# Kernel optimization log

Hardware: AMD Instinct MI355X
Metric: run time of the kernel (lower is better)

## Reference

```python
import jax, jax.numpy as jnp
import numpy as np

B, S, D = 2, 2048, 1024
NH, NKV, DH = 16, 4, 64
DFF, E, K, DE = 4096, 8, 2, 1024
CHUNK = 512
THETA = 10000.0
ROPE_PERIOD = 4  # int(1/(1-0.75))


def rmsnorm(x, gamma):
    den = jnp.sqrt(jnp.mean(x * x, axis=-1, keepdims=True) + 1e-6)
    return x / den * gamma


def apply_rope(x, base):
    # x: [b, s, h, d]
    s, d = x.shape[1], x.shape[3]
    m = jnp.arange(s, dtype=x.dtype)[:, None]                    # [s,1]
    i = jnp.arange(0, d, 2, dtype=x.dtype)
    theta = jnp.power(jnp.asarray(base, x.dtype), -i / d)        # [d/2]
    ang = (m * theta)[None, :, None, :]                          # [1,s,1,d/2]
    cos, sin = jnp.cos(ang), jnp.sin(ang)
    x1, x2 = x[..., 0::2], x[..., 1::2]
    r1 = x1 * cos - x2 * sin
    r2 = x1 * sin + x2 * cos
    return jnp.stack([r1, r2], axis=-1).reshape(x.shape)


def setup_inputs() -> dict:
    key = jax.random.key(0)
    ks = jax.random.split(key, 16)
    sc = 0.02
    inp = {
        "x": jax.random.normal(ks[0], (B, S, D), jnp.float32),
        "idx": 1,
        "gamma1": jnp.ones((D,), jnp.float32),
        "gamma2": jnp.ones((D,), jnp.float32),
        "q_gamma": jnp.ones((DH,), jnp.float32),
        "k_gamma": jnp.ones((DH,), jnp.float32),
        "w_q": jax.random.normal(ks[1], (D, NH * DH), jnp.float32) * sc,
        "w_k": jax.random.normal(ks[2], (D, NKV * DH), jnp.float32) * sc,
        "w_v": jax.random.normal(ks[3], (D, NKV * DH), jnp.float32) * sc,
        "w_o": jax.random.normal(ks[4], (D, D), jnp.float32) * sc,
        "w_router": jax.random.normal(ks[5], (D, E), jnp.float32) * sc,
        "sh_wg": jax.random.normal(ks[6], (D, DE), jnp.float32) * sc,
        "sh_wu": jax.random.normal(ks[7], (D, DE), jnp.float32) * sc,
        "sh_wd": jax.random.normal(ks[8], (DE, D), jnp.float32) * sc,
        "e_wg": jax.random.normal(ks[9], (E, D, DE), jnp.float32) * sc,
        "e_wu": jax.random.normal(ks[10], (E, D, DE), jnp.float32) * sc,
        "e_wd": jax.random.normal(ks[11], (E, DE, D), jnp.float32) * sc,
    }
    return inp


def reference(x, idx, gamma1, gamma2, q_gamma, k_gamma, w_q, w_k, w_v, w_o,
              w_router, sh_wg, sh_wu, sh_wd, e_wg, e_wu, e_wd):
    b, s, d = x.shape
    x_res = x
    h = rmsnorm(x, gamma1)

    # --- attention ---
    q = (h @ w_q).reshape(b, s, NH, DH)
    k = (h @ w_k).reshape(b, s, NKV, DH)
    v = (h @ w_v).reshape(b, s, NKV, DH)
    q = rmsnorm(q, q_gamma)
    k = rmsnorm(k, k_gamma)

    is_rope = (idx + 1) % ROPE_PERIOD != 0
    if is_rope:
        q = apply_rope(q, THETA)
        k = apply_rope(k, THETA)

    n_rep = NH // NKV
    k = jnp.repeat(k, n_rep, axis=2)  # [b,s,NH,DH]
    v = jnp.repeat(v, n_rep, axis=2)

    scores = jnp.einsum('bqhd,bkhd->bhqk', q, k) / np.sqrt(DH).astype(np.float32)

    pos = jnp.arange(s)
    if is_rope:
        same_chunk = (pos[:, None] // CHUNK) == (pos[None, :] // CHUNK)
        allowed = same_chunk & (pos[None, :] <= pos[:, None])
    else:
        allowed = pos[None, :] <= pos[:, None]
    scores = jnp.where(allowed[None, None], scores, -jnp.inf)
    attn = jax.nn.softmax(scores, axis=-1)
    out = jnp.einsum('bhqk,bkhd->bqhd', attn, v).reshape(b, s, d)
    x = out @ w_o + x_res

    # --- FFN ---
    x_res = x
    h = rmsnorm(x, gamma2)
    if idx % 2 == 0:
        raise NotImplementedError('dense layer path not exercised (idx odd)')
    # MoE: router + top-k combine (dense-weights formulation, same math)
    hf = h.reshape(-1, d)                           # [T, D]
    T = hf.shape[0]
    probs = jax.nn.softmax(hf @ w_router, axis=-1)  # [T, E]
    topw, topi = jax.lax.top_k(probs, K)
    topw = topw / jnp.sum(topw, axis=-1, keepdims=True)
    dense_w = jnp.zeros((T, E), hf.dtype).at[jnp.arange(T)[:, None], topi].add(topw)

    # shared expert
    sh = (jax.nn.silu(hf @ sh_wg) * (hf @ sh_wu)) @ sh_wd

    # all experts densely, weighted combine (zero-weight experts contribute 0)
    g = jax.nn.silu(jnp.einsum('td,edf->etf', hf, e_wg))
    u = jnp.einsum('td,edf->etf', hf, e_wu)
    eo = jnp.einsum('etf,efd->etd', g * u, e_wd)    # [E, T, D]
    moe = jnp.einsum('te,etd->td', dense_w, eo) + sh

    return moe.reshape(b, s, d) + x_res
```

## Files before the change

### kernel.cpp

```cpp
#include <hip/hip_runtime.h>
#include <hip/hip_bf16.h>

#define TS    2048
#define TT    4096
#define TCHUNK 512

typedef __bf16 bf16;
typedef __bf16 bf16x8 __attribute__((ext_vector_type(8)));
typedef __bf16 bf16x4 __attribute__((ext_vector_type(4)));
typedef float  f32x4  __attribute__((ext_vector_type(4)));

#define QPL ((size_t)TT*1024)
#define KPL ((size_t)TT*256)
#define VPL ((size_t)8*64*TS)
#define APL ((size_t)TT*1024)
#define H1PL ((size_t)TT*1024)

__device__ __forceinline__ f32x4 mfma16(bf16x8 a, bf16x8 b, f32x4 c){
  return __builtin_amdgcn_mfma_f32_16x16x32_bf16(a, b, c, 0, 0, 0);
}
__device__ __forceinline__ void gload_lds16(const void* g, void* lds){
  __builtin_amdgcn_global_load_lds(
      (const __attribute__((address_space(1))) unsigned int*)g,
      (__attribute__((address_space(3))) unsigned int*)lds, 16, 0, 0);
}
__device__ __forceinline__ void split2f(float x, bf16& h, bf16& m){
  h = (bf16)x; m = (bf16)(x - (float)h);
}

__global__ __launch_bounds__(256) void tcvt2_all_k(const float* __restrict__ wq, const float* __restrict__ wk,
                                                   const float* __restrict__ wv, const float* __restrict__ wo,
                                                   bf16* __restrict__ wqkv2, bf16* __restrict__ wo2){
  int z = blockIdx.z;
  const float* src; bf16* dst; int C; long pl, doff;
  if (z==0){ src=wq; dst=wqkv2; C=1024; pl=(long)1536*1024; doff=0; }
  else if (z==1){ src=wk; dst=wqkv2; C=256; pl=(long)1536*1024; doff=(long)1024*1024; }
  else if (z==2){ src=wv; dst=wqkv2; C=256; pl=(long)1536*1024; doff=(long)1280*1024; }
  else { src=wo; dst=wo2; C=1024; pl=(long)1024*1024; doff=0; }
  int c0 = blockIdx.x*32;
  if (c0 >= C) return;
  __shared__ float tile[32][33];
  int r0 = blockIdx.y*32;
  int tx = threadIdx.x, ty = threadIdx.y;
  #pragma unroll
  for (int i=0;i<4;i++)
    tile[ty+i*8][tx] = src[(size_t)(r0+ty+i*8)*C + c0+tx];
  __syncthreads();
  #pragma unroll
  for (int i=0;i<4;i++){
    float v = tile[tx][ty+i*8];
    bf16 h,m; split2f(v,h,m);
    size_t o = doff + (size_t)(c0+ty+i*8)*1024 + r0+tx;
    dst[o] = h; dst[pl + o] = m;
  }
}

__global__ __launch_bounds__(256) void tcvt_moe_k(const float* __restrict__ shwg, const float* __restrict__ shwu,
                                                  const float* __restrict__ shwd, const float* __restrict__ ewg,
                                                  const float* __restrict__ ewu, const float* __restrict__ ewd,
                                                  bf16* __restrict__ shwgu, bf16* __restrict__ shwd_t,
                                                  bf16* __restrict__ ewgu, bf16* __restrict__ ewd_t){
  int z = blockIdx.z;
  const float* src; bf16* dst; int mode;
  if (z==0){ src=shwg; dst=shwgu; mode=0; }
  else if (z==1){ src=shwu; dst=shwgu; mode=1; }
  else if (z==2){ src=shwd; dst=shwd_t; mode=2; }
  else if (z<11){ int e=z-3;  src=ewg+(size_t)e*1048576; dst=ewgu+(size_t)e*2097152; mode=0; }
  else if (z<19){ int e=z-11; src=ewu+(size_t)e*1048576; dst=ewgu+(size_t)e*2097152; mode=1; }
  else          { int e=z-19; src=ewd+(size_t)e*1048576; dst=ewd_t+(size_t)e*1048576; mode=2; }
  __shared__ float tile[32][33];
  int r0 = blockIdx.y*32, c0 = blockIdx.x*32;
  int tx = threadIdx.x, ty = threadIdx.y;
  #pragma unroll
  for (int i=0;i<4;i++)
    tile[ty+i*8][tx] = src[(size_t)(r0+ty+i*8)*1024 + c0+tx];
  __syncthreads();
  #pragma unroll
  for (int i=0;i<4;i++){
    int c = c0+ty+i*8;
    int orow = (mode==2) ? c : ((c>>4)*32 + (c&15) + (mode==1?16:0));
    dst[(size_t)orow*1024 + r0+tx] = (bf16)tile[tx][ty+i*8];
  }
}

__global__ __launch_bounds__(256) void rmsnorm2_k(const float* __restrict__ x, const float* __restrict__ g,
                                                  bf16* __restrict__ o2){
  int row = blockIdx.x, tid = threadIdx.x, wid = tid>>6, lane = tid&63;
  f32x4 v = ((const f32x4*)(x + (size_t)row*1024))[tid];
  float ss = v[0]*v[0]+v[1]*v[1]+v[2]*v[2]+v[3]*v[3];
  #pragma unroll
  for (int m=1;m<64;m<<=1) ss += __shfl_xor(ss, m);
  __shared__ float red[4];
  if (lane==0) red[wid] = ss;
  __syncthreads();
  float tot = red[0]+red[1]+red[2]+red[3];
  float inv = rsqrtf(tot*(1.f/1024.f) + 1e-6f);
  f32x4 gv = ((const f32x4*)g)[tid];
  #pragma unroll
  for (int i=0;i<4;i++){
    float val = v[i]*inv*gv[i];
    bf16 h,m; split2f(val,h,m);
    size_t idx = (size_t)row*1024 + tid*4 + i;
    o2[idx] = h; o2[H1PL + idx] = m;
  }
}

template<int OUT, int GATHER, int GROUPED>
__global__ __launch_bounds__(256) void gemm_k(
    const bf16* __restrict__ Aptr, int lda,
    const bf16* __restrict__ Bt, long bMatStride,
    void* __restrict__ Cout, int ldc,
    const float* __restrict__ resid,
    const int* __restrict__ gidx,
    const int* __restrict__ grpBase,
    const int* __restrict__ grpCnt,
    int M, int K){
  int tid = threadIdx.x;
  int wid = tid >> 6, lane = tid & 63;
  int lr = lane & 15, lg = lane >> 4;
  int e = blockIdx.z;
  int base = GROUPED ? grpBase[e] : 0;
  int cnt  = GROUPED ? grpCnt[e]  : M;
  int m0, bn0;
  if (GROUPED){
    m0 = blockIdx.y * 128;
    bn0 = blockIdx.x * 128;
  } else {
    int gx = gridDim.x;
    int bid = blockIdx.y*gx + blockIdx.x;
    int cpx = (gx*gridDim.y)>>3;
    int swz = (bid&7)*cpx + (bid>>3);
    m0 = (swz/gx) * 128;
    bn0 = (swz%gx) * 128;
  }
  if (m0 >= cnt) return;
  const bf16* Bte = Bt + (size_t)e * bMatStride;

  __shared__ __align__(16) bf16 As[128*32];
  __shared__ __align__(16) bf16 Bs[128*32];

  int rA0 = tid >> 2, colA = (tid & 3) * 8;
  long arow[2], brow[2];
  #pragma unroll
  for (int i=0;i<2;i++){
    int r = rA0 + i*64;
    int ar = m0 + r; if (ar > cnt-1) ar = cnt-1;
    arow[i] = GATHER ? (long)gidx[base + ar] : (long)(base + ar);
    brow[i] = bn0 + r;
  }

  f32x4 zero4 = {0.f,0.f,0.f,0.f};
  f32x4 acc[4][4];
  #pragma unroll
  for (int m=0;m<4;m++)
    #pragma unroll
    for (int n=0;n<4;n++) acc[m][n] = zero4;

  char* ldsA = (char*)As + wid*1024;
  char* ldsB = (char*)Bs + wid*1024;
  int wr = (wid>>1)*64, wc = (wid&1)*64;

  for (int k0 = 0; k0 < K; k0 += 32){
    #pragma unroll
    for (int i=0;i<2;i++){
      gload_lds16(Aptr + arow[i]*lda + k0 + colA, ldsA + i*4096);
      gload_lds16(Bte  + brow[i]*K   + k0 + colA, ldsB + i*4096);
    }
    asm volatile("s_waitcnt vmcnt(0)" ::: "memory");
    __syncthreads();
    bf16x8 af[4], bfr[4];
    #pragma unroll
    for (int m=0;m<4;m++) af[m]  = *(const bf16x8*)&As[(wr + m*16 + lr)*32 + lg*8];
    #pragma unroll
    for (int n=0;n<4;n++) bfr[n] = *(const bf16x8*)&Bs[(wc + n*16 + lr)*32 + lg*8];
    #pragma unroll
    for (int m=0;m<4;m++)
      #pragma unroll
      for (int n=0;n<4;n++)
        acc[m][n] = mfma16(af[m], bfr[n], acc[m][n]);
    __syncthreads();
  }
  #pragma unroll
  for (int m=0;m<4;m++){
    #pragma unroll
    for (int j=0;j<4;j++){
      int gr = m0 + wr + m*16 + lg*4 + j;
      if (gr < cnt){
        size_t orow = (size_t)(base + gr);
        if (OUT==2){
          #pragma unroll
          for (int np=0;np<2;np++){
            float gv = acc[m][2*np][j], uv = acc[m][2*np+1][j];
            float ov = gv * uv / (1.f + __expf(-gv));
            int f = ((bn0+wc)>>1) + np*16 + lr;
            ((bf16*)Cout)[orow*ldc + f] = (bf16)ov;
          }
        } else {
          #pragma unroll
          for (int n=0;n<4;n++){
            int gc = bn0 + wc + n*16 + lr;
            float v = acc[m][n][j];
            if (OUT==1){
              ((bf16*)Cout)[orow*ldc + gc] = (bf16)v;
            } else {
              ((float*)Cout)[orow*ldc + gc] = v + resid[orow*ldc + gc];
            }
          }
        }
      }
    }
  }
}

template<int RESID>
__global__ __launch_bounds__(256) void gemm2_k(
    const bf16* __restrict__ A2, long aPL, int lda,
    const bf16* __restrict__ B2, long bPL, int K,
    float* __restrict__ C, int ldc,
    const float* __restrict__ resid){
  int tid = threadIdx.x;
  int wid = tid >> 6, lane = tid & 63;
  int lr = lane & 15, lg = lane >> 4;
  int gx = gridDim.x;
  int bid = blockIdx.y*gx + blockIdx.x;
  int cpx = (gx*gridDim.y)>>3;
  int swz = (bid&7)*cpx + (bid>>3);
  int m0 = (swz/gx) * 128;
  int bn0 = (swz%gx) * 128;

  __shared__ __align__(16) bf16 As[2*128*32];
  __shared__ __align__(16) bf16 Bs[2*128*32];

  int rA0 = tid >> 2, colA = (tid & 3) * 8;
  f32x4 zero4 = {0.f,0.f,0.f,0.f};
  f32x4 acc[4][4];
  #pragma unroll
  for (int m=0;m<4;m++)
    #pragma unroll
    for (int n=0;n<4;n++) acc[m][n] = zero4;

  int wr = (wid>>1)*64, wc = (wid&1)*64;

  for (int k0 = 0; k0 < K; k0 += 32){
    #pragma unroll
    for (int p=0;p<2;p++){
      #pragma unroll
      for (int i=0;i<2;i++){
        int r = rA0 + i*64;
        gload_lds16(A2 + (size_t)p*aPL + (size_t)(m0 + r)*lda + k0 + colA,
                    (char*)As + p*8192 + wid*1024 + i*4096);
        gload_lds16(B2 + (size_t)p*bPL + (size_t)(bn0 + r)*K + k0 + colA,
                    (char*)Bs + p*8192 + wid*1024 + i*4096);
      }
    }
    asm volatile("s_waitcnt vmcnt(0)" ::: "memory");
    __syncthreads();
    bf16x8 af[2][4], bfr[2][4];
    #pragma unroll
    for (int p=0;p<2;p++){
      #pragma unroll
      for (int m=0;m<4;m++) af[p][m]  = *(const bf16x8*)&As[p*4096 + (wr + m*16 + lr)*32 + lg*8];
      #pragma unroll
      for (int n=0;n<4;n++) bfr[p][n] = *(const bf16x8*)&Bs[p*4096 + (wc + n*16 + lr)*32 + lg*8];
    }
    #pragma unroll
    for (int m=0;m<4;m++)
      #pragma unroll
      for (int n=0;n<4;n++){
        f32x4 a = acc[m][n];
        a = mfma16(af[0][m], bfr[0][n], a);
        a = mfma16(af[0][m], bfr[1][n], a);
        a = mfma16(af[1][m], bfr[0][n], a);
        a = mfma16(af[1][m], bfr[1][n], a);
        acc[m][n] = a;
      }
    __syncthreads();
  }
  #pragma unroll
  for (int m=0;m<4;m++){
    #pragma unroll
    for (int j=0;j<4;j++){
      size_t orow = (size_t)(m0 + wr + m*16 + lg*4 + j);
      #pragma unroll
      for (int n=0;n<4;n++){
        int gc = bn0 + wc + n*16 + lr;
        float v = acc[m][n][j];
        if (RESID) v += resid[orow*ldc + gc];
        C[orow*ldc + gc] = v;
      }
    }
  }
}

__global__ __launch_bounds__(256) void rope2_k(const float* __restrict__ qkv, bf16* __restrict__ Q2,
                                               bf16* __restrict__ K2, const int* __restrict__ idxp,
                                               const float* __restrict__ qg, const float* __restrict__ kg){
  int tid = threadIdx.x, wid = tid>>6, lane = tid&63;
  int u = blockIdx.x*4 + wid;
  int t = u / 20, r = u % 20;
  bool isq = (r < 16);
  int srcOff = isq ? r*64 : 1024 + (r-16)*64;
  float val = qkv[(size_t)t*1536 + srcOff + lane];
  float ss = val*val;
  #pragma unroll
  for (int m=1;m<64;m<<=1) ss += __shfl_xor(ss, m);
  float inv = rsqrtf(ss*(1.f/64.f) + 1e-6f);
  const float* gm = isq ? qg : kg;
  val = val * inv * gm[lane];
  bool rope = ((idxp[0] + 1) % 4) != 0;
  if (rope){
    int s = t & (TS-1);
    float fi = (float)(lane & ~1);
    float theta = (float)exp((double)fi * -0.14391156831212787);
    float ang = (float)s * theta;
    float sn, cs;
    sincosf(ang, &sn, &cs);
    float other = __shfl_xor(val, 1);
    val = (lane & 1) ? (other*sn + val*cs) : (val*cs - other*sn);
  }
  bf16 h,m2; split2f(val,h,m2);
  if (isq){
    size_t base = (size_t)t*1024 + r*64 + lane;
    Q2[base] = h; Q2[QPL + base] = m2;
  } else {
    size_t base = (size_t)t*256 + (r-16)*64 + lane;
    K2[base] = h; K2[KPL + base] = m2;
  }
}

__global__ __launch_bounds__(256) void vtrans2_k(const float* __restrict__ src, bf16* __restrict__ dst){
  __shared__ float tile[32][33];
  int z = blockIdx.z;
  const float* s = src + (size_t)(z>>2)*((size_t)TS*1536) + (z&3)*64 + 1280;
  int r0 = blockIdx.y*32, c0 = blockIdx.x*32;
  int tx = threadIdx.x, ty = threadIdx.y;
  #pragma unroll
  for (int i=0;i<4;i++)
    tile[ty+i*8][tx] = s[(size_t)(r0+ty+i*8)*1536 + c0+tx];
  __syncthreads();
  size_t zb = (size_t)z*(64*TS);
  #pragma unroll
  for (int i=0;i<4;i++){
    float v = tile[tx][ty+i*8];
    bf16 h,m; split2f(v,h,m);
    size_t o = zb + (size_t)(c0+ty+i*8)*TS + r0+tx;
    dst[o] = h; dst[VPL + o] = m;
  }
}

__global__ __launch_bounds__(256) void attn2_k(const bf16* __restrict__ Q2, const bf16* __restrict__ K2,
                                               const bf16* __restrict__ V2, bf16* __restrict__ A2,
                                               const int* __restrict__ idxp){
  int tid = threadIdx.x, wid = tid>>6, lane = tid&63;
  int lr = lane&15, lg = lane>>4;
  int flat = (blockIdx.z*gridDim.y + blockIdx.y)*gridDim.x + blockIdx.x;
  int swz = (flat&7)*128 + (flat>>3);
  int qt = swz & 31, h = (swz>>5)&15, b = swz>>9;
  int kvh = h >> 2;
  int q0 = qt*64;
  bool rope = ((idxp[0]+1) % 4) != 0;
  int kstart = rope ? (q0 / TCHUNK) * TCHUNK : 0;
  int ntiles = (q0 + 64 - kstart) >> 5;

  __shared__ __align__(16) bf16 Ks[2*32*64];
  __shared__ __align__(16) bf16 Vs[2*64*32];
  __shared__ __align__(16) bf16 Ps[4][2][16*32];

  bf16x8 qf[2][2];
  {
    size_t qrow = (size_t)(b*TS + q0 + wid*16 + lr);
    #pragma unroll
    for (int p=0;p<2;p++)
      #pragma unroll
      for (int kf=0;kf<2;kf++)
        qf[p][kf] = *(const bf16x8*)&Q2[(size_t)p*QPL + qrow*1024 + h*64 + kf*32 + lg*8];
  }

  int krow = tid>>3;
  int kcb  = (tid&7) ^ (krow&7);
  int vrow = tid>>2;
  int vcb  = tid&3;

  f32x4 o[4];
  f32x4 zero4 = {0.f,0.f,0.f,0.f};
  #pragma unroll
  for (int n=0;n<4;n++) o[n] = zero4;
  float mrow[4], lrow[4];
  #pragma unroll
  for (int j=0;j<4;j++){ mrow[j] = -1e30f; lrow[j] = 0.f; }

  for (int kt=0; kt<ntiles; kt++){
    int kt0 = kstart + kt*32;
    #pragma unroll
    for (int p=0;p<2;p++){
      gload_lds16(K2 + (size_t)p*KPL + ((size_t)(b*TS + kt0 + krow))*256 + kvh*64 + kcb*8,
                  (char*)Ks + p*4096 + wid*1024);
      gload_lds16(V2 + (size_t)p*VPL + ((size_t)((b*4 + kvh)*64 + vrow))*TS + kt0 + vcb*8,
                  (char*)Vs + p*4096 + wid*1024);
    }
    asm volatile("s_waitcnt vmcnt(0)" ::: "memory");
    __syncthreads();

    f32x4 sc[2];
    #pragma unroll
    for (int cf=0; cf<2; cf++){
      int r = cf*16 + lr;
      int sw = (lr&7) << 3;
      bf16x8 kh0 = *(const bf16x8*)&Ks[0*2048 + r*64 + (((lg  )<<3) ^ sw)];
      bf16x8 kh1 = *(const bf16x8*)&Ks[0*2048 + r*64 + (((lg+4)<<3) ^ sw)];
      bf16x8 km0 = *(const bf16x8*)&Ks[1*2048 + r*64 + (((lg  )<<3) ^ sw)];
      bf16x8 km1 = *(const bf16x8*)&Ks[1*2048 + r*64 + (((lg+4)<<3) ^ sw)];
      f32x4 a = zero4;
      a = mfma16(qf[0][0], kh0, a); a = mfma16(qf[0][1], kh1, a);
      a = mfma16(qf[0][0], km0, a); a = mfma16(qf[0][1], km1, a);
      a = mfma16(qf[1][0], kh0, a); a = mfma16(qf[1][1], kh1, a);
      a = mfma16(qf[1][0], km0, a); a = mfma16(qf[1][1], km1, a);
      sc[cf] = a;
    }
    #pragma unroll
    for (int j=0;j<4;j++){
      int qtok = q0 + wid*16 + lg*4 + j;
      float pmax = -1e30f;
      #pragma unroll
      for (int cf=0;cf<2;cf++){
        int ktok = kt0 + cf*16 + lr;
        float sv = (ktok <= qtok) ? sc[cf][j]*0.125f : -1e30f;
        sc[cf][j] = sv;
        pmax = fmaxf(pmax, sv);
      }
      #pragma unroll
      for (int m=1;m<16;m<<=1) pmax = fmaxf(pmax, __shfl_xor(pmax, m));
      float mnew = fmaxf(mrow[j], pmax);
      float corr = __expf(mrow[j]-mnew);
      float psum = 0.f;
      #pragma unroll
      for (int cf=0;cf<2;cf++){
        float p = __expf(sc[cf][j]-mnew);
        sc[cf][j] = p;
        psum += p;
      }
      #pragma unroll
      for (int m=1;m<16;m<<=1) psum += __shfl_xor(psum, m);
      lrow[j] = lrow[j]*corr + psum;
      mrow[j] = mnew;
      #pragma unroll
      for (int n=0;n<4;n++) o[n][j] *= corr;
      #pragma unroll
      for (int cf=0;cf<2;cf++){
        float p = sc[cf][j];
        bf16 ph = (bf16)p;
        bf16 pl = (bf16)(p - (float)ph);
        int pidx = (lg*4+j)*32 + cf*16 + lr;
        Ps[wid][0][pidx] = ph;
        Ps[wid][1][pidx] = pl;
      }
    }
    __syncthreads();
    bf16x8 pa0 = *(const bf16x8*)&Ps[wid][0][lr*32 + lg*8];
    bf16x8 pa1 = *(const bf16x8*)&Ps[wid][1][lr*32 + lg*8];
    #pragma unroll
    for (int n=0;n<4;n++){
      bf16x8 vh = *(const bf16x8*)&Vs[0*2048 + (n*16+lr)*32 + lg*8];
      bf16x8 vm = *(const bf16x8*)&Vs[1*2048 + (n*16+lr)*32 + lg*8];
      f32x4 a = o[n];
      a = mfma16(pa0, vh, a);
      a = mfma16(pa0, vm, a);
      a = mfma16(pa1, vh, a);
      a = mfma16(pa1, vm, a);
      o[n] = a;
    }
    __syncthreads();
  }
  #pragma unroll
  for (int j=0;j<4;j++){
    int qtok = q0 + wid*16 + lg*4 + j;
    float invl = 1.f / lrow[j];
    size_t rowb = ((size_t)(b*TS + qtok))*1024 + h*64;
    #pragma unroll
    for (int n=0;n<4;n++){
      float v = o[n][j]*invl;
      bf16 h2,m2; split2f(v,h2,m2);
      size_t oidx = rowb + n*16 + lr;
      A2[oidx] = h2; A2[APL + oidx] = m2;
    }
  }
}

__global__ __launch_bounds__(256) void rmsrouter_k(const float* __restrict__ x2, const float* __restrict__ g2,
                                                   const float* __restrict__ wr, bf16* __restrict__ h2,
                                                   int* __restrict__ topi, float* __restrict__ topw){
  int tid = threadIdx.x, wid = tid>>6, lane = tid&63;
  int t = blockIdx.x*4 + wid;
  const float* row = x2 + (size_t)t*1024;
  f32x4 xv[4];
  float ss = 0.f;
  #pragma unroll
  for (int j=0;j<4;j++){
    xv[j] = ((const f32x4*)row)[lane + j*64];
    ss += xv[j][0]*xv[j][0]+xv[j][1]*xv[j][1]+xv[j][2]*xv[j][2]+xv[j][3]*xv[j][3];
  }
  #pragma unroll
  for (int m=1;m<64;m<<=1) ss += __shfl_xor(ss, m);
  float inv = 1.f / sqrtf(ss*(1.f/1024.f) + 1e-6f);
  float a[8] = {0,0,0,0,0,0,0,0};
  #pragma unroll
  for (int j=0;j<4;j++){
    bf16x4 hb;
    #pragma unroll
    for (int c=0;c<4;c++){
      int d = (lane + j*64)*4 + c;
      float hv = xv[j][c]*inv*g2[d];
      hb[c] = (bf16)hv;
      f32x4 wa = ((const f32x4*)(wr + (size_t)d*8))[0];
      f32x4 wb = ((const f32x4*)(wr + (size_t)d*8))[1];
      a[0]+=hv*wa[0]; a[1]+=hv*wa[1]; a[2]+=hv*wa[2]; a[3]+=hv*wa[3];
      a[4]+=hv*wb[0]; a[5]+=hv*wb[1]; a[6]+=hv*wb[2]; a[7]+=hv*wb[3];
    }
    *(bf16x4*)(h2 + (size_t)t*1024 + (lane + j*64)*4) = hb;
  }
  #pragma unroll
  for (int e2=0;e2<8;e2++)
    #pragma unroll
    for (int m=1;m<64;m<<=1) a[e2] += __shfl_xor(a[e2], m);
  if (lane==0){
    int i0=0; float l0=a[0];
    #pragma unroll
    for (int e2=1;e2<8;e2++) if (a[e2] > l0){ l0=a[e2]; i0=e2; }
    int i1=-1; float l1=-1e30f;
    #pragma unroll
    for (int e2=0;e2<8;e2++){ if (e2==i0) continue; if (a[e2] > l1){ l1=a[e2]; i1=e2; } }
    float w0 = 1.f/(1.f + __expf(l1 - l0));
    topi[t*2]=i0; topi[t*2+1]=i1;
    topw[t*2]=w0; topw[t*2+1]=1.f-w0;
  }
}

__global__ __launch_bounds__(1024) void route_build_k(const int* __restrict__ topi, int* __restrict__ rowsb,
                                                      int* __restrict__ t2p, int* __restrict__ cntp,
                                                      int* __restrict__ basep){
  __shared__ int wcnt[16][8], wbase[16][8], wcur[16][8];
  int tid = threadIdx.x, w = tid>>6;
  if (tid < 128){ wcnt[tid>>3][tid&7]=0; wcur[tid>>3][tid&7]=0; }
  __syncthreads();
  for (int i=tid; i<TT*2; i+=1024) atomicAdd(&wcnt[w][topi[i]], 1);
  __syncthreads();
  if (tid==0){
    int run=0;
    for (int e=0;e<8;e++){
      basep[e]=run; int s=run;
      for (int ww=0;ww<16;ww++){ wbase[ww][e]=run; run+=wcnt[ww][e]; }
      cntp[e]=run-s;
    }
  }
  __syncthreads();
  for (int i=tid; i<TT*2; i+=1024){
    int e = topi[i];
    int p = wbase[w][e] + atomicAdd(&wcur[w][e], 1);
    rowsb[p] = i>>1;
    t2p[i] = p;
  }
}

__global__ void combine_k(const float* __restrict__ acc, const bf16* __restrict__ eo,
                          const float* __restrict__ topw, const int* __restrict__ t2p,
                          float* __restrict__ out){
  int i = blockIdx.x*256 + threadIdx.x;
  int t = i >> 8, c = (i & 255)*4;
  int p0 = t2p[t*2], p1 = t2p[t*2+1];
  float w0 = topw[t*2], w1 = topw[t*2+1];
  f32x4 a = *(const f32x4*)&acc[(size_t)t*1024 + c];
  bf16x4 e0 = *(const bf16x4*)&eo[(size_t)p0*1024 + c];
  bf16x4 e1 = *(const bf16x4*)&eo[(size_t)p1*1024 + c];
  f32x4 r;
  #pragma unroll
  for (int k=0;k<4;k++) r[k] = a[k] + w0*(float)e0[k] + w1*(float)e1[k];
  *(f32x4*)&out[(size_t)t*1024 + c] = r;
}

extern "C" void kernel_launch(void* const* d_in, const int* in_sizes, int n_in,
                              void* d_out, int out_size, void* d_ws, size_t ws_size,
                              hipStream_t stream){
  const float* x        = (const float*)d_in[0];
  const int*   idx      = (const int*)d_in[1];
  const float* gamma1   = (const float*)d_in[2];
  const float* gamma2   = (const float*)d_in[3];
  const float* qg       = (const float*)d_in[4];
  const float* kg       = (const float*)d_in[5];
  const float* w_q      = (const float*)d_in[6];
  const float* w_k      = (const float*)d_in[7];
  const float* w_v      = (const float*)d_in[8];
  const float* w_o      = (const float*)d_in[9];
  const float* w_router = (const float*)d_in[10];
  const float* sh_wg    = (const float*)d_in[11];
  const float* sh_wu    = (const float*)d_in[12];
  const float* sh_wd    = (const float*)d_in[13];
  const float* e_wg     = (const float*)d_in[14];
  const float* e_wu     = (const float*)d_in[15];
  const float* e_wd     = (const float*)d_in[16];
  float* out = (float*)d_out;

  char* ws = (char*)d_ws;
  size_t off = 0;
  auto alloc = [&](size_t n)->char*{ char* p = ws + off; off += (n + 255) & ~(size_t)255; return p; };

  const long PLQKV = (long)1536*1024;
  const long PLSQ  = (long)1024*1024;

  bf16* wqkv2  = (bf16*)alloc((size_t)2*1536*1024*2);
  bf16* wo2    = (bf16*)alloc((size_t)2*1024*1024*2);
  bf16* shwgu_t= (bf16*)alloc((size_t)2048*1024*2);
  bf16* shwd_t = (bf16*)alloc((size_t)1024*1024*2);
  bf16* ewgu_t = (bf16*)alloc((size_t)8*2048*1024*2);
  bf16* ewd_t  = (bf16*)alloc((size_t)8*1024*1024*2);
  bf16* h1s    = (bf16*)alloc((size_t)2*TT*1024*2);
  float* qkvraw= (float*)alloc((size_t)TT*1536*4);
  bf16* q2     = (bf16*)alloc((size_t)2*TT*1024*2);
  bf16* k2     = (bf16*)alloc((size_t)2*TT*256*2);
  bf16* v2     = (bf16*)alloc((size_t)2*8*64*TS*2);
  float* x2    = (float*)alloc((size_t)TT*1024*4);
  float* accb  = (float*)alloc((size_t)TT*1024*4);
  char* BUF2   = alloc((size_t)8192*1024*2);
  bf16* eo     = (bf16*)alloc((size_t)8192*1024*2);
  int*   topi  = (int*)alloc((size_t)TT*2*4);
  float* topw  = (float*)alloc((size_t)TT*2*4);
  int*   rowsb = (int*)alloc((size_t)TT*2*4);
  int*   t2p   = (int*)alloc((size_t)TT*2*4);
  int*   cntp  = (int*)alloc(256);
  int*   basep = (int*)alloc(256);
  (void)ws_size; (void)in_sizes; (void)n_in; (void)out_size;

  bf16* a2     = (bf16*)qkvraw;
  bf16* h2     = q2;
  bf16* shg    = (bf16*)BUF2;
  bf16* gu     = (bf16*)BUF2;

  dim3 tb(32,8);
  tcvt2_all_k<<<dim3(32,32,4), tb, 0, stream>>>(w_q, w_k, w_v, w_o, wqkv2, wo2);
  tcvt_moe_k<<<dim3(32,32,27), tb, 0, stream>>>(sh_wg, sh_wu, sh_wd, e_wg, e_wu, e_wd,
                                                shwgu_t, shwd_t, ewgu_t, ewd_t);

  rmsnorm2_k<<<TT, 256, 0, stream>>>(x, gamma1, h1s);
  gemm2_k<0><<<dim3(12,32,1), 256, 0, stream>>>(h1s, (long)H1PL, 1024, wqkv2, PLQKV, 1024,
                                                qkvraw, 1536, nullptr);
  rope2_k<<<TT*20/4, 256, 0, stream>>>(qkvraw, q2, k2, idx, qg, kg);
  vtrans2_k<<<dim3(2,64,8), tb, 0, stream>>>(qkvraw, v2);
  attn2_k<<<dim3(32,16,2), 256, 0, stream>>>(q2, k2, v2, a2, idx);
  gemm2_k<1><<<dim3(8,32,1), 256, 0, stream>>>(a2, (long)APL, 1024, wo2, PLSQ, 1024,
                                               x2, 1024, x);
  rmsrouter_k<<<TT/4, 256, 0, stream>>>(x2, gamma2, w_router, h2, topi, topw);
  route_build_k<<<1, 1024, 0, stream>>>(topi, rowsb, t2p, cntp, basep);
  gemm_k<2,0,0><<<dim3(16,32,1), 256, 0, stream>>>(h2,1024, shwgu_t,0, shg,1024,
                                                   nullptr, nullptr, nullptr, nullptr, TT, 1024);
  gemm_k<0,0,0><<<dim3(8,32,1), 256, 0, stream>>>(shg,1024, shwd_t,0, accb,1024,
                                                  x2, nullptr, nullptr, nullptr, TT, 1024);
  gemm_k<2,1,1><<<dim3(16,64,8), 256, 0, stream>>>(h2,1024, ewgu_t,(long)2048*1024, gu,1024,
                                                   nullptr, rowsb, basep, cntp, TT, 1024);
  gemm_k<1,0,1><<<dim3(8,64,8), 256, 0, stream>>>(gu,1024, ewd_t,(long)1024*1024, eo,1024,
                                                  nullptr, nullptr, basep, cntp, TT, 1024);
  combine_k<<<TT, 256, 0, stream>>>(accb, eo, topw, t2p, out);
}
```

Baseline: 429.9 us.

## Fold shared expert into grouped MoE GEMMs and drop low-order split MFMAs

Treats the shared expert as a ninth expert group covering all tokens: its weights sit after the routed experts, rowsb gains an identity segment, and the grouped GEMMs launch with nine z-slices. This removes two separate shared-expert GEMM launches and the fp32 accumulation buffer, and the combine kernel adds the shared output. Separately, it drops the lo*lo term of the split-bf16 products in the QKV/O GEMMs and both attention matmuls, cutting MFMA work at a small precision cost. The shared-expert output is now stored as bf16 instead of fp32 with the residual added, which adds rounding.

```diff
diff --git a/kernel.cpp b/kernel.cpp
--- a/kernel.cpp
+++ b/kernel.cpp
@@ -199,12 +199,7 @@
           #pragma unroll
           for (int n=0;n<4;n++){
             int gc = bn0 + wc + n*16 + lr;
-            float v = acc[m][n][j];
-            if (OUT==1){
-              ((bf16*)Cout)[orow*ldc + gc] = (bf16)v;
-            } else {
-              ((float*)Cout)[orow*ldc + gc] = v + resid[orow*ldc + gc];
-            }
+            ((bf16*)Cout)[orow*ldc + gc] = (bf16)acc[m][n][j];
           }
         }
       }
@@ -271,7 +266,6 @@
         a = mfma16(af[0][m], bfr[0][n], a);
         a = mfma16(af[0][m], bfr[1][n], a);
         a = mfma16(af[1][m], bfr[0][n], a);
-        a = mfma16(af[1][m], bfr[1][n], a);
         acc[m][n] = a;
       }
     __syncthreads();
@@ -414,7 +408,6 @@
       a = mfma16(qf[0][0], kh0, a); a = mfma16(qf[0][1], kh1, a);
       a = mfma16(qf[0][0], km0, a); a = mfma16(qf[0][1], km1, a);
       a = mfma16(qf[1][0], kh0, a); a = mfma16(qf[1][1], kh1, a);
-      a = mfma16(qf[1][0], km0, a); a = mfma16(qf[1][1], km1, a);
       sc[cf] = a;
     }
     #pragma unroll
@@ -466,7 +459,6 @@
       a = mfma16(pa0, vh, a);
       a = mfma16(pa0, vm, a);
       a = mfma16(pa1, vh, a);
-      a = mfma16(pa1, vm, a);
       o[n] = a;
     }
     __syncthreads();
@@ -551,6 +543,7 @@
       for (int ww=0;ww<16;ww++){ wbase[ww][e]=run; run+=wcnt[ww][e]; }
       cntp[e]=run-s;
     }
+    basep[8]=TT*2; cntp[8]=TT;
   }
   __syncthreads();
   for (int i=tid; i<TT*2; i+=1024){
@@ -559,21 +552,23 @@
     rowsb[p] = i>>1;
     t2p[i] = p;
   }
-}
-
-__global__ void combine_k(const float* __restrict__ acc, const bf16* __restrict__ eo,
+  for (int i=tid; i<TT; i+=1024) rowsb[TT*2+i] = i;
+}
+
+__global__ void combine_k(const float* __restrict__ x2, const bf16* __restrict__ eo,
                           const float* __restrict__ topw, const int* __restrict__ t2p,
                           float* __restrict__ out){
   int i = blockIdx.x*256 + threadIdx.x;
   int t = i >> 8, c = (i & 255)*4;
   int p0 = t2p[t*2], p1 = t2p[t*2+1];
   float w0 = topw[t*2], w1 = topw[t*2+1];
-  f32x4 a = *(const f32x4*)&acc[(size_t)t*1024 + c];
+  f32x4 a = *(const f32x4*)&x2[(size_t)t*1024 + c];
   bf16x4 e0 = *(const bf16x4*)&eo[(size_t)p0*1024 + c];
   bf16x4 e1 = *(const bf16x4*)&eo[(size_t)p1*1024 + c];
+  bf16x4 es = *(const bf16x4*)&eo[((size_t)(TT*2) + t)*1024 + c];
   f32x4 r;
   #pragma unroll
-  for (int k=0;k<4;k++) r[k] = a[k] + w0*(float)e0[k] + w1*(float)e1[k];
+  for (int k=0;k<4;k++) r[k] = a[k] + (float)es[k] + w0*(float)e0[k] + w1*(float)e1[k];
   *(f32x4*)&out[(size_t)t*1024 + c] = r;
 }
 
@@ -608,31 +603,28 @@
 
   bf16* wqkv2  = (bf16*)alloc((size_t)2*1536*1024*2);
   bf16* wo2    = (bf16*)alloc((size_t)2*1024*1024*2);
-  bf16* shwgu_t= (bf16*)alloc((size_t)2048*1024*2);
-  bf16* shwd_t = (bf16*)alloc((size_t)1024*1024*2);
-  bf16* ewgu_t = (bf16*)alloc((size_t)8*2048*1024*2);
-  bf16* ewd_t  = (bf16*)alloc((size_t)8*1024*1024*2);
+  bf16* ewgu_t = (bf16*)alloc((size_t)9*2048*1024*2);
+  bf16* ewd_t  = (bf16*)alloc((size_t)9*1024*1024*2);
   bf16* h1s    = (bf16*)alloc((size_t)2*TT*1024*2);
   float* qkvraw= (float*)alloc((size_t)TT*1536*4);
   bf16* q2     = (bf16*)alloc((size_t)2*TT*1024*2);
   bf16* k2     = (bf16*)alloc((size_t)2*TT*256*2);
   bf16* v2     = (bf16*)alloc((size_t)2*8*64*TS*2);
   float* x2    = (float*)alloc((size_t)TT*1024*4);
-  float* accb  = (float*)alloc((size_t)TT*1024*4);
-  char* BUF2   = alloc((size_t)8192*1024*2);
-  bf16* eo     = (bf16*)alloc((size_t)8192*1024*2);
+  bf16* gu     = (bf16*)alloc((size_t)(TT*3)*1024*2);
+  bf16* eo     = (bf16*)alloc((size_t)(TT*3)*1024*2);
   int*   topi  = (int*)alloc((size_t)TT*2*4);
   float* topw  = (float*)alloc((size_t)TT*2*4);
-  int*   rowsb = (int*)alloc((size_t)TT*2*4);
+  int*   rowsb = (int*)alloc((size_t)TT*3*4);
   int*   t2p   = (int*)alloc((size_t)TT*2*4);
   int*   cntp  = (int*)alloc(256);
   int*   basep = (int*)alloc(256);
   (void)ws_size; (void)in_sizes; (void)n_in; (void)out_size;
 
-  bf16* a2     = (bf16*)qkvraw;
-  bf16* h2     = q2;
-  bf16* shg    = (bf16*)BUF2;
-  bf16* gu     = (bf16*)BUF2;
+  bf16* shwgu_t = ewgu_t + (size_t)8*2048*1024;
+  bf16* shwd_t  = ewd_t  + (size_t)8*1024*1024;
+  bf16* a2      = (bf16*)qkvraw;
+  bf16* h2      = q2;
 
   dim3 tb(32,8);
   tcvt2_all_k<<<dim3(32,32,4), tb, 0, stream>>>(w_q, w_k, w_v, w_o, wqkv2, wo2);
@@ -649,13 +641,9 @@
                                                x2, 1024, x);
   rmsrouter_k<<<TT/4, 256, 0, stream>>>(x2, gamma2, w_router, h2, topi, topw);
   route_build_k<<<1, 1024, 0, stream>>>(topi, rowsb, t2p, cntp, basep);
-  gemm_k<2,0,0><<<dim3(16,32,1), 256, 0, stream>>>(h2,1024, shwgu_t,0, shg,1024,
-                                                   nullptr, nullptr, nullptr, nullptr, TT, 1024);
-  gemm_k<0,0,0><<<dim3(8,32,1), 256, 0, stream>>>(shg,1024, shwd_t,0, accb,1024,
-                                                  x2, nullptr, nullptr, nullptr, TT, 1024);
-  gemm_k<2,1,1><<<dim3(16,64,8), 256, 0, stream>>>(h2,1024, ewgu_t,(long)2048*1024, gu,1024,
+  gemm_k<2,1,1><<<dim3(16,64,9), 256, 0, stream>>>(h2,1024, ewgu_t,(long)2048*1024, gu,1024,
                                                    nullptr, rowsb, basep, cntp, TT, 1024);
-  gemm_k<1,0,1><<<dim3(8,64,8), 256, 0, stream>>>(gu,1024, ewd_t,(long)1024*1024, eo,1024,
+  gemm_k<1,0,1><<<dim3(8,64,9), 256, 0, stream>>>(gu,1024, ewd_t,(long)1024*1024, eo,1024,
                                                   nullptr, nullptr, basep, cntp, TT, 1024);
-  combine_k<<<TT, 256, 0, stream>>>(accb, eo, topw, t2p, out);
-}
+  combine_k<<<TT, 256, 0, stream>>>(x2, eo, topw, t2p, out);
+}
```

Result: faster. 407.5 us (-5.2%).
